# Kernel optimization log

Hardware: AMD Instinct MI355X
Metric: run time of the kernel (lower is better)

The kernel has to match this reference:

```python
import jax, jax.numpy as jnp
import numpy as np

DIM = 1024        # model dim
HEADS = 1         # num_heads (fc1 in_features==1 forces this)
HDIM = DIM // HEADS
INNER = 16        # dim_inner
B, L = 2, 4096
ROPE_BASE = 32.0


def _apply_rope(x, pos, base):
    # x: [b, l, h, d]; standard rotate-half RoPE
    d = x.shape[-1]
    inv_freq = base ** (-jnp.arange(0, d, 2, dtype=jnp.float32) / d)   # [d/2]
    ang = pos[:, None].astype(jnp.float32) * inv_freq                  # [l, d/2]
    emb = jnp.concatenate([ang, ang], axis=-1)                         # [l, d]
    cos = jnp.cos(emb)[None, :, None, :].astype(x.dtype)
    sin = jnp.sin(emb)[None, :, None, :].astype(x.dtype)
    x1, x2 = x[..., : d // 2], x[..., d // 2:]
    rot = jnp.concatenate([-x2, x1], axis=-1)
    return x * cos + rot * sin


def setup_inputs() -> dict:
    key = jax.random.key(0)
    ks = jax.random.split(key, 7)
    hidden_states = jax.random.normal(ks[0], (B, L, DIM), dtype=jnp.float32)
    Wq = jax.random.normal(ks[1], (DIM, DIM), dtype=jnp.float32) * 0.02
    Wk = jax.random.normal(ks[2], (DIM, DIM), dtype=jnp.float32) * 0.02
    fc1_w = jax.random.normal(ks[3], (INNER, 1), dtype=jnp.float32) * 0.1
    fc1_b = jax.random.normal(ks[4], (INNER,), dtype=jnp.float32) * 0.1
    fc2_w = jax.random.normal(ks[5], (DIM, INNER), dtype=jnp.float32) * 0.1
    fc2_b = jax.random.normal(ks[6], (DIM,), dtype=jnp.float32) * 0.1
    return {"hidden_states": hidden_states, "Wq": Wq, "Wk": Wk,
            "fc1_w": fc1_w, "fc1_b": fc1_b, "fc2_w": fc2_w, "fc2_b": fc2_b}


def reference(hidden_states, Wq, Wk, fc1_w, fc1_b, fc2_w, fc2_b):
    b, l, _ = hidden_states.shape
    # projections, cast to bf16 as in the torch module
    q = (hidden_states @ Wq.T).reshape(b, l, HEADS, HDIM).astype(jnp.bfloat16)
    k = (hidden_states @ Wk.T).reshape(b, l, HEADS, HDIM).astype(jnp.bfloat16)
    pos = jnp.arange(l)
    q = _apply_rope(q, pos, ROPE_BASE)
    k = _apply_rope(k, pos, ROPE_BASE)
    # causal exp(QK) with NO softmax normalization; accumulate in fp32
    scores = jnp.einsum('bqhd,bkhd->bhqk',
                        q.astype(jnp.float32), k.astype(jnp.float32)) / (HDIM ** 0.5)
    causal = jnp.tril(jnp.ones((l, l), dtype=bool))                    # [l, l]
    exp_qk = jnp.where(causal[None, None], jnp.exp(scores), 0.0)       # [b, h, l, l]
    o = jnp.swapaxes(exp_qk.sum(axis=-1), 1, 2)                        # [b, l, h]
    # small MLP: h(=1) -> INNER -> DIM
    o = jax.nn.relu(o @ fc1_w.T + fc1_b)
    return o @ fc2_w.T + fc2_b                                         # [b, l, DIM]
```

## Files before the change

kernel.cpp:

```cpp
#include <hip/hip_runtime.h>
#include <hip/hip_bf16.h>

typedef __bf16 bf16_t;
typedef __bf16 bf16x4 __attribute__((ext_vector_type(4)));
typedef __bf16 bf16x8 __attribute__((ext_vector_type(8)));
typedef float f32x4 __attribute__((ext_vector_type(4)));

#define B_   2
#define L_   4096
#define DIM_ 1024
#define M_   (B_ * L_)
#define NTASK2_ 272

__device__ __forceinline__ void ld_g2l_16(const bf16_t* g, bf16_t* l) {
  __builtin_amdgcn_global_load_lds(
      (__attribute__((address_space(1))) void*)g,
      (__attribute__((address_space(3))) void*)l, 16, 0, 0);
}

__global__ void cvt_all(const float* __restrict__ hs, const float* __restrict__ wq,
                        const float* __restrict__ wk, bf16_t* __restrict__ hs_b,
                        bf16_t* __restrict__ wq_b, bf16_t* __restrict__ wk_b,
                        float* __restrict__ o) {
  const int N_HS = M_ * DIM_ / 4, N_W = DIM_ * DIM_ / 4;
  int i = blockIdx.x * blockDim.x + threadIdx.x;
  if (i < M_ / 4) ((float4*)o)[i] = float4{0.f, 0.f, 0.f, 0.f};
  const float* s; bf16_t* d; int idx;
  if (i < N_HS)            { s = hs; d = hs_b; idx = i; }
  else if (i < N_HS + N_W) { s = wq; d = wq_b; idx = i - N_HS; }
  else                     { s = wk; d = wk_b; idx = i - N_HS - N_W; }
  float4 v = ((const float4*)s)[idx];
  bf16x4 ov = { (bf16_t)v.x, (bf16_t)v.y, (bf16_t)v.z, (bf16_t)v.w };
  ((bf16x4*)d)[idx] = ov;
}

template <int BSEGS>
__device__ __forceinline__ void core256(const bf16_t* __restrict__ A,
                                        const bf16_t* __restrict__ B0,
                                        const bf16_t* __restrict__ B1,
                                        bf16_t* sm, bool active,
                                        f32x4 (&acc)[4][BSEGS / 2]) {
  constexpr int SEGS = 16 + BSEGS;
  constexpr int BUF  = SEGS * 512;
  const int tid  = threadIdx.x;
  const int wave = tid >> 6, lane = tid & 63;
  const int wm = wave >> 1, wn = wave & 1;
  const int quad = lane >> 4, l16 = lane & 15;
  const int srow = lane >> 2;
  const int scol = (((lane & 3) ^ ((lane >> 3) & 3)) * 8);
  const int rsw  = ((l16 >> 1) & 3) * 8;
  const int loff = l16 * 32 + ((quad * 8) ^ rsw);

  const bf16_t* gA0 = A + (size_t)(wave * 16 + srow) * DIM_ + scol;
  const bf16_t* gA1 = A + (size_t)((wave + 8) * 16 + srow) * DIM_ + scol;
  const bf16_t* gB0 = B0 + (size_t)(wave * 16 + srow) * DIM_ + scol;
  const bf16_t* gB1 = gB0;
  if constexpr (BSEGS == 16) gB1 = B1 + (size_t)(wave * 16 + srow) * DIM_ + scol;

  bf16_t* pb0 = sm;
  bf16_t* pb1 = sm + BUF;

  auto stage = [&](int kk, bf16_t* buf) {
    ld_g2l_16(gA0 + kk, buf + wave * 512);
    ld_g2l_16(gA1 + kk, buf + (wave + 8) * 512);
    ld_g2l_16(gB0 + kk, buf + (16 + wave) * 512);
    if constexpr (BSEGS == 16) ld_g2l_16(gB1 + kk, buf + (24 + wave) * 512);
  };

  stage(0, pb0);
  stage(32, pb1);
  if constexpr (BSEGS == 16) asm volatile("s_waitcnt vmcnt(4)" ::: "memory");
  else                       asm volatile("s_waitcnt vmcnt(3)" ::: "memory");
  __builtin_amdgcn_s_barrier();
  __builtin_amdgcn_sched_barrier(0);

  for (int s = 0; s < 32; ++s) {
    bf16_t* cur = (s & 1) ? pb1 : pb0;
    bf16x8 aF[4], bF[BSEGS / 2];
    if (active) {
#pragma unroll
      for (int rf = 0; rf < 4; ++rf)
        aF[rf] = *(const bf16x8*)(cur + (wm * 4 + rf) * 512 + loff);
#pragma unroll
      for (int cf = 0; cf < BSEGS / 2; ++cf) {
        int k = (cf & 3) + wn * 4 + (cf >> 2) * 8;
        bF[cf] = *(const bf16x8*)(cur + (16 + k) * 512 + loff);
      }
    }
    asm volatile("s_waitcnt lgkmcnt(0)" ::: "memory");
    __builtin_amdgcn_sched_barrier(0);
    __builtin_amdgcn_s_barrier();
    __builtin_amdgcn_sched_barrier(0);
    if (s + 2 < 32) stage((s + 2) * 32, cur);
    if (active) {
      __builtin_amdgcn_s_setprio(1);
#pragma unroll
      for (int rf = 0; rf < 4; ++rf)
#pragma unroll
        for (int cf = 0; cf < BSEGS / 2; ++cf)
          acc[rf][cf] = __builtin_amdgcn_mfma_f32_16x16x32_bf16(
              aF[rf], bF[cf], acc[rf][cf], 0, 0, 0);
      __builtin_amdgcn_s_setprio(0);
    }
    if (s < 30) {
      if constexpr (BSEGS == 16) asm volatile("s_waitcnt vmcnt(4)" ::: "memory");
      else                       asm volatile("s_waitcnt vmcnt(3)" ::: "memory");
    } else if (s == 30) {
      asm volatile("s_waitcnt vmcnt(0)" ::: "memory");
    }
    __builtin_amdgcn_s_barrier();
    __builtin_amdgcn_sched_barrier(0);
  }
}

__global__ __launch_bounds__(512, 2)
void proj_gemm(const bf16_t* __restrict__ A, const bf16_t* __restrict__ Wqb,
               const bf16_t* __restrict__ Wkb, bf16_t* __restrict__ Cq,
               bf16_t* __restrict__ Ck) {
  __shared__ __attribute__((aligned(16))) bf16_t sm[2 * 32 * 512];
  int logical = ((blockIdx.x & 7) << 5) | (blockIdx.x >> 3);
  int zn = logical >> 5;
  int z = zn >> 2, n0 = (zn & 3) * 128;
  int m0 = (logical & 31) * 256;
  const bf16_t* Wb = z ? Wkb : Wqb;
  bf16_t* Cm = z ? Ck : Cq;

  f32x4 acc[4][8] = {};
  core256<16>(A + (size_t)m0 * DIM_, Wb + (size_t)n0 * DIM_,
              Wb + (size_t)(n0 + 512) * DIM_, sm, true, acc);

  const int tid = threadIdx.x, wave = tid >> 6, lane = tid & 63;
  const int wm = wave >> 1, wn = wave & 1;
  const int quad = lane >> 4, l16 = lane & 15;

  float inv[4];
#pragma unroll
  for (int cf = 0; cf < 4; ++cf) {
    int j = n0 + wn * 64 + cf * 16 + l16;
    inv[cf] = exp2f((float)j * (-5.0f / 512.0f));
  }
#pragma unroll
  for (int rf = 0; rf < 4; ++rf)
#pragma unroll
    for (int r = 0; r < 4; ++r) {
      int m = m0 + wm * 64 + rf * 16 + quad * 4 + r;
      float posf = (float)(m & (L_ - 1));
#pragma unroll
      for (int cf = 0; cf < 4; ++cf) {
        int j = n0 + wn * 64 + cf * 16 + l16;
        float ang = posf * inv[cf];
        float c = cosf(ang), s = sinf(ang);
        float cb = (float)(bf16_t)c, sb = (float)(bf16_t)s;
        float x1 = (float)(bf16_t)acc[rf][cf][r];
        float x2 = (float)(bf16_t)acc[rf][cf + 4][r];
        Cm[(size_t)m * DIM_ + j]       = (bf16_t)(x1 * cb - x2 * sb);
        Cm[(size_t)m * DIM_ + j + 512] = (bf16_t)(x2 * cb + x1 * sb);
      }
    }
}

__global__ __launch_bounds__(512, 4)
void attn_rowsum(const bf16_t* __restrict__ Q, const bf16_t* __restrict__ Kc,
                 float* __restrict__ o) {
  __shared__ __attribute__((aligned(16))) bf16_t sm[2 * 24 * 512];
  int logical = (blockIdx.x & 7) * 68 + (blockIdx.x >> 3);
  int b = logical / NTASK2_;
  int t = logical - b * NTASK2_;
  int mi = (int)((sqrtf(4.0f * (float)t + 1.0f) - 1.0f) * 0.5f);
  while ((mi + 1) * (mi + 2) <= t) ++mi;
  while (mi * (mi + 1) > t) --mi;
  int nt = t - mi * (mi + 1);

  const int tid = threadIdx.x, wave = tid >> 6, lane = tid & 63;
  const int wm = wave >> 1, wn = wave & 1;
  const int quad = lane >> 4, l16 = lane & 15;

  const bf16_t* A  = Q  + (size_t)b * L_ * DIM_ + (size_t)mi * 256 * DIM_;
  const bf16_t* Bp = Kc + (size_t)b * L_ * DIM_ + (size_t)nt * 128 * DIM_;

  bool active = (mi * 256 + wm * 64 + 63) >= nt * 128;

  f32x4 acc[4][4] = {};
  core256<8>(A, Bp, nullptr, sm, active, acc);

  if (active) {
    const bool masked = (nt >= 2 * mi);
#pragma unroll
    for (int rf = 0; rf < 4; ++rf) {
#pragma unroll
      for (int r = 0; r < 4; ++r) {
        int grow = mi * 256 + wm * 64 + rf * 16 + quad * 4 + r;
        float sum = 0.0f;
#pragma unroll
        for (int cf = 0; cf < 4; ++cf) {
          int gcol = nt * 128 + wn * 64 + cf * 16 + l16;
          float e = __expf(acc[rf][cf][r] * 0.03125f);
          if (!masked || gcol <= grow) sum += e;
        }
        sum += __shfl_xor(sum, 1);
        sum += __shfl_xor(sum, 2);
        sum += __shfl_xor(sum, 4);
        sum += __shfl_xor(sum, 8);
        if (l16 == 0)
          atomicAdd(&o[b * L_ + grow], sum);
      }
    }
  }
}

__global__ __launch_bounds__(256)
void mlp_out_kernel(const float* __restrict__ o, const float* __restrict__ fc1_w,
                    const float* __restrict__ fc1_b, const float* __restrict__ fc2_w,
                    const float* __restrict__ fc2_b, float* __restrict__ out) {
  const int R = 16;
  int row0 = blockIdx.x * R;
  int tid = threadIdx.x;
  __shared__ float h[R][16];
  {
    int rl = tid >> 4, i = tid & 15;
    float s = o[row0 + rl];
    h[rl][i] = fmaxf(fc1_w[i] * s + fc1_b[i], 0.0f);
  }
  __syncthreads();
  int d = tid * 4;
  float w[4][16];
#pragma unroll
  for (int c = 0; c < 4; ++c)
#pragma unroll
    for (int i = 0; i < 16; ++i) w[c][i] = fc2_w[(d + c) * 16 + i];
  float4 bb = *(const float4*)(fc2_b + d);
  for (int rl = 0; rl < R; ++rl) {
    float4 v = bb;
#pragma unroll
    for (int i = 0; i < 16; ++i) {
      float hv = h[rl][i];
      v.x += w[0][i] * hv; v.y += w[1][i] * hv;
      v.z += w[2][i] * hv; v.w += w[3][i] * hv;
    }
    *(float4*)(out + (size_t)(row0 + rl) * DIM_ + d) = v;
  }
}

extern "C" void kernel_launch(void* const* d_in, const int* in_sizes, int n_in,
                              void* d_out, int out_size, void* d_ws, size_t ws_size,
                              hipStream_t stream) {
  const float* hs    = (const float*)d_in[0];
  const float* Wq    = (const float*)d_in[1];
  const float* Wk    = (const float*)d_in[2];
  const float* fc1_w = (const float*)d_in[3];
  const float* fc1_b = (const float*)d_in[4];
  const float* fc2_w = (const float*)d_in[5];
  const float* fc2_b = (const float*)d_in[6];
  float* out = (float*)d_out;

  char* ws = (char*)d_ws;
  bf16_t* hs_bf = (bf16_t*)ws; ws += (size_t)M_ * DIM_ * 2;
  bf16_t* wq_bf = (bf16_t*)ws; ws += (size_t)DIM_ * DIM_ * 2;
  bf16_t* wk_bf = (bf16_t*)ws; ws += (size_t)DIM_ * DIM_ * 2;
  bf16_t* q_bf  = (bf16_t*)ws; ws += (size_t)M_ * DIM_ * 2;
  bf16_t* k_bf  = (bf16_t*)ws; ws += (size_t)M_ * DIM_ * 2;
  float*  o     = (float*)ws;

  const int n4 = (M_ * DIM_ + 2 * DIM_ * DIM_) / 4;
  cvt_all<<<n4 / 256, 256, 0, stream>>>(hs, Wq, Wk, hs_bf, wq_bf, wk_bf, o);

  proj_gemm<<<256, 512, 0, stream>>>(hs_bf, wq_bf, wk_bf, q_bf, k_bf);

  attn_rowsum<<<544, 512, 0, stream>>>(q_bf, k_bf, o);

  mlp_out_kernel<<<M_ / 16, 256, 0, stream>>>(o, fc1_w, fc1_b, fc2_w, fc2_b, out);
}
```

Baseline: 261.5 us.

## Fuse MLP into attention rowsum via completion counters, stage GEMM epilogue through LDS

The separate MLP kernel is removed. Each row-block of attention now counts finished column tiles with an atomic counter, and the last tile to finish computes the MLP output for its 256 rows. The projection GEMM now writes its RoPE output through LDS so global stores become coalesced 16-byte writes. Both kernels also get new tile-to-block mappings for XCD locality. The cost is a serialized MLP tail in the last block of each row group, plus extra fences and atomics.

```diff
diff --git a/kernel.cpp b/kernel.cpp
--- a/kernel.cpp
+++ b/kernel.cpp
@@ -21,10 +21,11 @@
 __global__ void cvt_all(const float* __restrict__ hs, const float* __restrict__ wq,
                         const float* __restrict__ wk, bf16_t* __restrict__ hs_b,
                         bf16_t* __restrict__ wq_b, bf16_t* __restrict__ wk_b,
-                        float* __restrict__ o) {
+                        float* __restrict__ o, int* __restrict__ cnt) {
   const int N_HS = M_ * DIM_ / 4, N_W = DIM_ * DIM_ / 4;
   int i = blockIdx.x * blockDim.x + threadIdx.x;
   if (i < M_ / 4) ((float4*)o)[i] = float4{0.f, 0.f, 0.f, 0.f};
+  if (i < 8) ((int4*)cnt)[i] = int4{0, 0, 0, 0};
   const float* s; bf16_t* d; int idx;
   if (i < N_HS)            { s = hs; d = hs_b; idx = i; }
   else if (i < N_HS + N_W) { s = wq; d = wq_b; idx = i - N_HS; }
@@ -117,11 +118,12 @@
 void proj_gemm(const bf16_t* __restrict__ A, const bf16_t* __restrict__ Wqb,
                const bf16_t* __restrict__ Wkb, bf16_t* __restrict__ Cq,
                bf16_t* __restrict__ Ck) {
-  __shared__ __attribute__((aligned(16))) bf16_t sm[2 * 32 * 512];
-  int logical = ((blockIdx.x & 7) << 5) | (blockIdx.x >> 3);
-  int zn = logical >> 5;
-  int z = zn >> 2, n0 = (zn & 3) * 128;
-  int m0 = (logical & 31) * 256;
+  __shared__ __attribute__((aligned(16))) bf16_t sm[256 * 136];
+  const int bid = blockIdx.x;
+  const int xcd = bid & 7, slot = bid >> 3;
+  const int m0 = (xcd * 4 + (slot >> 3)) * 256;
+  const int zn = slot & 7;
+  const int z = zn >> 2, n0 = (zn & 3) * 128;
   const bf16_t* Wb = z ? Wkb : Wqb;
   bf16_t* Cm = z ? Ck : Cq;
 
@@ -139,37 +141,67 @@
     int j = n0 + wn * 64 + cf * 16 + l16;
     inv[cf] = exp2f((float)j * (-5.0f / 512.0f));
   }
-#pragma unroll
-  for (int rf = 0; rf < 4; ++rf)
-#pragma unroll
-    for (int r = 0; r < 4; ++r) {
-      int m = m0 + wm * 64 + rf * 16 + quad * 4 + r;
-      float posf = (float)(m & (L_ - 1));
-#pragma unroll
-      for (int cf = 0; cf < 4; ++cf) {
-        int j = n0 + wn * 64 + cf * 16 + l16;
-        float ang = posf * inv[cf];
-        float c = cosf(ang), s = sinf(ang);
-        float cb = (float)(bf16_t)c, sb = (float)(bf16_t)s;
-        float x1 = (float)(bf16_t)acc[rf][cf][r];
-        float x2 = (float)(bf16_t)acc[rf][cf + 4][r];
-        Cm[(size_t)m * DIM_ + j]       = (bf16_t)(x1 * cb - x2 * sb);
-        Cm[(size_t)m * DIM_ + j + 512] = (bf16_t)(x2 * cb + x1 * sb);
+
+#pragma unroll 1
+  for (int g = 0; g < 2; ++g) {
+    __syncthreads();
+#pragma unroll
+    for (int rf = 0; rf < 4; ++rf)
+#pragma unroll
+      for (int r = 0; r < 4; ++r) {
+        int row = wm * 64 + rf * 16 + quad * 4 + r;
+        float posf = (float)((m0 + row) & (L_ - 1));
+#pragma unroll
+        for (int cf = 0; cf < 4; ++cf) {
+          int col = wn * 64 + cf * 16 + l16;
+          float ang = posf * inv[cf];
+          float c = cosf(ang), s = sinf(ang);
+          float cb = (float)(bf16_t)c, sb = (float)(bf16_t)s;
+          float x1 = (float)(bf16_t)acc[rf][cf][r];
+          float x2 = (float)(bf16_t)acc[rf][cf + 4][r];
+          float v = g ? (x2 * cb + x1 * sb) : (x1 * cb - x2 * sb);
+          sm[row * 136 + col] = (bf16_t)v;
+        }
       }
-    }
+    __syncthreads();
+#pragma unroll
+    for (int it = 0; it < 8; ++it) {
+      int row = it * 32 + (tid >> 4);
+      int c8  = (tid & 15) * 8;
+      bf16x8 v = *(const bf16x8*)(sm + row * 136 + c8);
+      *(bf16x8*)(Cm + (size_t)(m0 + row) * DIM_ + n0 + g * 512 + c8) = v;
+    }
+  }
 }
 
 __global__ __launch_bounds__(512, 4)
 void attn_rowsum(const bf16_t* __restrict__ Q, const bf16_t* __restrict__ Kc,
-                 float* __restrict__ o) {
+                 float* o, int* cnt,
+                 const float* __restrict__ fc1_w, const float* __restrict__ fc1_b,
+                 const float* __restrict__ fc2_w, const float* __restrict__ fc2_b,
+                 float* __restrict__ out) {
   __shared__ __attribute__((aligned(16))) bf16_t sm[2 * 24 * 512];
-  int logical = (blockIdx.x & 7) * 68 + (blockIdx.x >> 3);
-  int b = logical / NTASK2_;
-  int t = logical - b * NTASK2_;
-  int mi = (int)((sqrtf(4.0f * (float)t + 1.0f) - 1.0f) * 0.5f);
-  while ((mi + 1) * (mi + 2) <= t) ++mi;
-  while (mi * (mi + 1) > t) --mi;
-  int nt = t - mi * (mi + 1);
+  __shared__ int lastdone;
+  const int bid = blockIdx.x;
+  const int xcd = bid & 7, slot = bid >> 3;
+  const int l = xcd * 68 + slot;
+  const int b = (l >= NTASK2_) ? 1 : 0;
+  const int t = l - b * NTASK2_;
+
+  int g = (t >= 156) ? 3 : (t >= 72) ? 2 : (t >= 20) ? 1 : 0;
+  int u = t - (16 * g * g + 4 * g);
+  int mi, nt;
+  if (u < 32 * g) {
+    int nb = u >> 5, v = u & 31;
+    mi = 4 * g + (v >> 3);
+    nt = nb * 8 + (v & 7);
+  } else {
+    int up = u - 32 * g;
+    if (up < 2)       { mi = 4 * g;     nt = 8 * g + up; }
+    else if (up < 6)  { mi = 4 * g + 1; nt = 8 * g + up - 2; }
+    else if (up < 12) { mi = 4 * g + 2; nt = 8 * g + up - 6; }
+    else              { mi = 4 * g + 3; nt = 8 * g + up - 12; }
+  }
 
   const int tid = threadIdx.x, wave = tid >> 6, lane = tid & 63;
   const int wm = wave >> 1, wn = wave & 1;
@@ -206,38 +238,38 @@
       }
     }
   }
-}
-
-__global__ __launch_bounds__(256)
-void mlp_out_kernel(const float* __restrict__ o, const float* __restrict__ fc1_w,
-                    const float* __restrict__ fc1_b, const float* __restrict__ fc2_w,
-                    const float* __restrict__ fc2_b, float* __restrict__ out) {
-  const int R = 16;
-  int row0 = blockIdx.x * R;
-  int tid = threadIdx.x;
-  __shared__ float h[R][16];
-  {
-    int rl = tid >> 4, i = tid & 15;
-    float s = o[row0 + rl];
-    h[rl][i] = fmaxf(fc1_w[i] * s + fc1_b[i], 0.0f);
-  }
+
+  __threadfence();
   __syncthreads();
-  int d = tid * 4;
-  float w[4][16];
-#pragma unroll
-  for (int c = 0; c < 4; ++c)
-#pragma unroll
-    for (int i = 0; i < 16; ++i) w[c][i] = fc2_w[(d + c) * 16 + i];
-  float4 bb = *(const float4*)(fc2_b + d);
-  for (int rl = 0; rl < R; ++rl) {
-    float4 v = bb;
-#pragma unroll
-    for (int i = 0; i < 16; ++i) {
-      float hv = h[rl][i];
-      v.x += w[0][i] * hv; v.y += w[1][i] * hv;
-      v.z += w[2][i] * hv; v.w += w[3][i] * hv;
-    }
-    *(float4*)(out + (size_t)(row0 + rl) * DIM_ + d) = v;
+  if (tid == 0) {
+    int old = atomicAdd(&cnt[b * 16 + mi], 1);
+    lastdone = (old == 2 * mi + 1);
+  }
+  __syncthreads();
+  if (lastdone) {
+    __threadfence();
+    const int m0r = b * L_ + mi * 256;
+    const int d = (tid & 255) * 4;
+    float f1w[16], f1b[16], w[4][16];
+#pragma unroll
+    for (int i = 0; i < 16; ++i) { f1w[i] = fc1_w[i]; f1b[i] = fc1_b[i]; }
+#pragma unroll
+    for (int c = 0; c < 4; ++c)
+#pragma unroll
+      for (int i = 0; i < 16; ++i) w[c][i] = fc2_w[(d + c) * 16 + i];
+    float4 bb = *(const float4*)(fc2_b + d);
+    for (int it = 0; it < 128; ++it) {
+      int row = m0r + it * 2 + (tid >> 8);
+      float s = o[row];
+      float4 v = bb;
+#pragma unroll
+      for (int i = 0; i < 16; ++i) {
+        float h = fmaxf(f1w[i] * s + f1b[i], 0.0f);
+        v.x += w[0][i] * h; v.y += w[1][i] * h;
+        v.z += w[2][i] * h; v.w += w[3][i] * h;
+      }
+      *(float4*)(out + (size_t)row * DIM_ + d) = v;
+    }
   }
 }
 
@@ -259,14 +291,14 @@
   bf16_t* wk_bf = (bf16_t*)ws; ws += (size_t)DIM_ * DIM_ * 2;
   bf16_t* q_bf  = (bf16_t*)ws; ws += (size_t)M_ * DIM_ * 2;
   bf16_t* k_bf  = (bf16_t*)ws; ws += (size_t)M_ * DIM_ * 2;
-  float*  o     = (float*)ws;
+  float*  o     = (float*)ws;  ws += (size_t)M_ * sizeof(float);
+  int*    cnt   = (int*)ws;
 
   const int n4 = (M_ * DIM_ + 2 * DIM_ * DIM_) / 4;
-  cvt_all<<<n4 / 256, 256, 0, stream>>>(hs, Wq, Wk, hs_bf, wq_bf, wk_bf, o);
+  cvt_all<<<n4 / 256, 256, 0, stream>>>(hs, Wq, Wk, hs_bf, wq_bf, wk_bf, o, cnt);
 
   proj_gemm<<<256, 512, 0, stream>>>(hs_bf, wq_bf, wk_bf, q_bf, k_bf);
 
-  attn_rowsum<<<544, 512, 0, stream>>>(q_bf, k_bf, o);
-
-  mlp_out_kernel<<<M_ / 16, 256, 0, stream>>>(o, fc1_w, fc1_b, fc2_w, fc2_b, out);
-}
+  attn_rowsum<<<544, 512, 0, stream>>>(q_bf, k_bf, o, cnt,
+                                       fc1_w, fc1_b, fc2_w, fc2_b, out);
+}
```

Result: slower. 583.6 us (+123.2%).

## Triple-buffer GEMM LDS pipeline, stage RoPE epilogue through LDS, remap blocks

Applied to the files above, without the earlier changes.

The shared GEMM core moves from double to triple buffering, which removes the mid-iteration barrier and lets the next stage's global-to-LDS loads be issued right after the fragment reads. The projection kernel now writes its RoPE epilogue into LDS and then emits coalesced 16-byte row stores, replacing scattered 2-byte global stores. It also changes the block-to-XCD mapping so that blocks sharing an M tile sit on the same XCD. The larger LDS footprint pushes attn_rowsum's launch bounds down from 4 to 2 blocks per SM, which may cost occupancy.

```diff
diff --git a/kernel.cpp b/kernel.cpp
--- a/kernel.cpp
+++ b/kernel.cpp
@@ -57,8 +57,9 @@
   const bf16_t* gB1 = gB0;
   if constexpr (BSEGS == 16) gB1 = B1 + (size_t)(wave * 16 + srow) * DIM_ + scol;
 
-  bf16_t* pb0 = sm;
-  bf16_t* pb1 = sm + BUF;
+  bf16_t* p0 = sm;
+  bf16_t* p1 = sm + BUF;
+  bf16_t* p2 = sm + 2 * BUF;
 
   auto stage = [&](int kk, bf16_t* buf) {
     ld_g2l_16(gA0 + kk, buf + wave * 512);
@@ -67,31 +68,27 @@
     if constexpr (BSEGS == 16) ld_g2l_16(gB1 + kk, buf + (24 + wave) * 512);
   };
 
-  stage(0, pb0);
-  stage(32, pb1);
+  stage(0, p0);
+  stage(32, p1);
   if constexpr (BSEGS == 16) asm volatile("s_waitcnt vmcnt(4)" ::: "memory");
   else                       asm volatile("s_waitcnt vmcnt(3)" ::: "memory");
   __builtin_amdgcn_s_barrier();
-  __builtin_amdgcn_sched_barrier(0);
 
   for (int s = 0; s < 32; ++s) {
-    bf16_t* cur = (s & 1) ? pb1 : pb0;
     bf16x8 aF[4], bF[BSEGS / 2];
     if (active) {
 #pragma unroll
       for (int rf = 0; rf < 4; ++rf)
-        aF[rf] = *(const bf16x8*)(cur + (wm * 4 + rf) * 512 + loff);
+        aF[rf] = *(const bf16x8*)(p0 + (wm * 4 + rf) * 512 + loff);
 #pragma unroll
       for (int cf = 0; cf < BSEGS / 2; ++cf) {
         int k = (cf & 3) + wn * 4 + (cf >> 2) * 8;
-        bF[cf] = *(const bf16x8*)(cur + (16 + k) * 512 + loff);
+        bF[cf] = *(const bf16x8*)(p0 + (16 + k) * 512 + loff);
       }
     }
+    if (s < 30) stage((s + 2) * 32, p2);
     asm volatile("s_waitcnt lgkmcnt(0)" ::: "memory");
     __builtin_amdgcn_sched_barrier(0);
-    __builtin_amdgcn_s_barrier();
-    __builtin_amdgcn_sched_barrier(0);
-    if (s + 2 < 32) stage((s + 2) * 32, cur);
     if (active) {
       __builtin_amdgcn_s_setprio(1);
 #pragma unroll
@@ -109,7 +106,7 @@
       asm volatile("s_waitcnt vmcnt(0)" ::: "memory");
     }
     __builtin_amdgcn_s_barrier();
-    __builtin_amdgcn_sched_barrier(0);
+    bf16_t* t0 = p0; p0 = p1; p1 = p2; p2 = t0;
   }
 }
 
@@ -117,11 +114,12 @@
 void proj_gemm(const bf16_t* __restrict__ A, const bf16_t* __restrict__ Wqb,
                const bf16_t* __restrict__ Wkb, bf16_t* __restrict__ Cq,
                bf16_t* __restrict__ Ck) {
-  __shared__ __attribute__((aligned(16))) bf16_t sm[2 * 32 * 512];
-  int logical = ((blockIdx.x & 7) << 5) | (blockIdx.x >> 3);
-  int zn = logical >> 5;
-  int z = zn >> 2, n0 = (zn & 3) * 128;
-  int m0 = (logical & 31) * 256;
+  __shared__ __attribute__((aligned(16))) bf16_t sm[3 * 32 * 512];
+  const int bid = blockIdx.x;
+  const int xcd = bid & 7, slot = bid >> 3;
+  const int m0 = (xcd * 4 + (slot >> 3)) * 256;
+  const int zn = slot & 7;
+  const int z = zn >> 2, n0 = (zn & 3) * 128;
   const bf16_t* Wb = z ? Wkb : Wqb;
   bf16_t* Cm = z ? Ck : Cq;
 
@@ -139,30 +137,43 @@
     int j = n0 + wn * 64 + cf * 16 + l16;
     inv[cf] = exp2f((float)j * (-5.0f / 512.0f));
   }
-#pragma unroll
-  for (int rf = 0; rf < 4; ++rf)
-#pragma unroll
-    for (int r = 0; r < 4; ++r) {
-      int m = m0 + wm * 64 + rf * 16 + quad * 4 + r;
-      float posf = (float)(m & (L_ - 1));
-#pragma unroll
-      for (int cf = 0; cf < 4; ++cf) {
-        int j = n0 + wn * 64 + cf * 16 + l16;
-        float ang = posf * inv[cf];
-        float c = cosf(ang), s = sinf(ang);
-        float cb = (float)(bf16_t)c, sb = (float)(bf16_t)s;
-        float x1 = (float)(bf16_t)acc[rf][cf][r];
-        float x2 = (float)(bf16_t)acc[rf][cf + 4][r];
-        Cm[(size_t)m * DIM_ + j]       = (bf16_t)(x1 * cb - x2 * sb);
-        Cm[(size_t)m * DIM_ + j + 512] = (bf16_t)(x2 * cb + x1 * sb);
+
+#pragma unroll 1
+  for (int g = 0; g < 2; ++g) {
+    __syncthreads();
+#pragma unroll
+    for (int rf = 0; rf < 4; ++rf)
+#pragma unroll
+      for (int r = 0; r < 4; ++r) {
+        int row = wm * 64 + rf * 16 + quad * 4 + r;
+        float posf = (float)((m0 + row) & (L_ - 1));
+#pragma unroll
+        for (int cf = 0; cf < 4; ++cf) {
+          int col = wn * 64 + cf * 16 + l16;
+          float ang = posf * inv[cf];
+          float c = cosf(ang), s = sinf(ang);
+          float cb = (float)(bf16_t)c, sb = (float)(bf16_t)s;
+          float x1 = (float)(bf16_t)acc[rf][cf][r];
+          float x2 = (float)(bf16_t)acc[rf][cf + 4][r];
+          float v = g ? (x2 * cb + x1 * sb) : (x1 * cb - x2 * sb);
+          sm[row * 136 + col] = (bf16_t)v;
+        }
       }
-    }
-}
-
-__global__ __launch_bounds__(512, 4)
+    __syncthreads();
+#pragma unroll
+    for (int it = 0; it < 8; ++it) {
+      int row = it * 32 + (tid >> 4);
+      int c8  = (tid & 15) * 8;
+      bf16x8 v = *(const bf16x8*)(sm + row * 136 + c8);
+      *(bf16x8*)(Cm + (size_t)(m0 + row) * DIM_ + n0 + g * 512 + c8) = v;
+    }
+  }
+}
+
+__global__ __launch_bounds__(512, 2)
 void attn_rowsum(const bf16_t* __restrict__ Q, const bf16_t* __restrict__ Kc,
                  float* __restrict__ o) {
-  __shared__ __attribute__((aligned(16))) bf16_t sm[2 * 24 * 512];
+  __shared__ __attribute__((aligned(16))) bf16_t sm[3 * 24 * 512];
   int logical = (blockIdx.x & 7) * 68 + (blockIdx.x >> 3);
   int b = logical / NTASK2_;
   int t = logical - b * NTASK2_;
```

After: 280.7 us. 7.4% more time.
